# Performance work log

Measured on AMD Instinct MI355X. Metric: run time of the kernel, lower is better.

Reference implementation:

```python
import jax, jax.numpy as jnp
import numpy as np

B, S, F, D, K = 4096, 64, 8, 64, 16  # batch_size, seq_len, input_size, d_model, knns


def setup_inputs() -> dict:
    key = jax.random.key(0)
    ks = jax.random.split(key, 3)
    return {
        "x": jax.random.normal(ks[0], (B, S, F), jnp.float32),
        "W_emb": jax.random.normal(ks[1], (F, D), jnp.float32) / np.sqrt(F),
        "b_emb": jnp.zeros((D,), jnp.float32),
        "W_proj": jax.random.normal(ks[2], (D, F), jnp.float32) / np.sqrt(D),
        "b_proj": jnp.zeros((F,), jnp.float32),
    }


def reference(x, W_emb, b_emb, W_proj, b_proj):
    # enc_embedding
    x_enc = x @ W_emb + b_emb                       # [B,S,D]
    x_re = x_enc.reshape(B, S * D)                  # flatten per sample
    # batch self-similarity
    attn = jnp.einsum('bl,cl->bc', x_re, x_re) / np.sqrt(D * S)
    diag = jnp.eye(B, dtype=bool)
    attn = jnp.where(diag, -jnp.inf, attn)
    scores = jax.nn.softmax(attn, axis=-1)          # [B,B]
    # einsum('bd,bc->bd', x_re, scores) == x_re * scores.sum(-1)
    x_rec = x_re * jnp.sum(scores, axis=-1, keepdims=True)
    x_rec = x_rec.reshape(B, S, D)
    x_rec_proj = x_rec @ W_proj + b_proj            # [B,S,F]
    # top-k neighbor gather
    _, top_idx = jax.lax.top_k(scores, K)           # [B,K] int32
    gathered = x_rec_proj[top_idx]                  # [B,K,S,F]
    diff_1 = jnp.mean(jnp.diff(gathered, axis=1) ** 2)
    diff_2 = jnp.mean(jnp.diff(gathered, axis=2) ** 2)
    loss = jnp.mean((x_rec_proj - x) ** 2) + diff_1 + diff_2  # var == 2
    return loss, x_rec_proj
```

## Files before the change

### kernel.cpp

```cpp
#include <hip/hip_runtime.h>
#include <math.h>

#define NB 4096
#define NS 64
#define NF 8
#define ND 64
#define KL 512
#define NK 16

typedef _Float16 half8 __attribute__((ext_vector_type(8)));
typedef float    f32x4 __attribute__((ext_vector_type(4)));

#define GLD16(src, dst) \
  __builtin_amdgcn_global_load_lds((const __attribute__((address_space(1))) void*)(src), \
                                   (__attribute__((address_space(3))) void*)(dst), 16, 0, 0)

#define WAITVM(N) asm volatile("s_waitcnt vmcnt(" #N ")" ::: "memory")

__device__ __forceinline__ unsigned short f2bf_rne(float f) {
    unsigned v = __float_as_uint(f);
    return (unsigned short)((v + 0x7FFFu + ((v >> 16) & 1u)) >> 16);
}
__device__ __forceinline__ unsigned bf16key(float v, int col) {
    const unsigned u = f2bf_rne(v);
    const unsigned s = (u & 0x8000u) ? (~u & 0xFFFFu) : (u | 0x8000u);
    return (s << 12) | (unsigned)(4095 - col);
}

#define UPD2(M1, M2, K) { const unsigned k_ = (K); \
    if (k_ > M1) { M2 = M1; M1 = k_; } else if (k_ > M2) M2 = k_; }

__device__ __forceinline__ float blk_reduce(float v, float* red) {
    #pragma unroll
    for (int o = 32; o > 0; o >>= 1) v += __shfl_down(v, o, 64);
    const int t = threadIdx.x;
    __syncthreads();
    if ((t & 63) == 0) red[t >> 6] = v;
    __syncthreads();
    float r = 0.f;
    if (t == 0) r = red[0] + red[1] + red[2] + red[3];
    return r;
}

__global__ __launch_bounds__(64) void consts_kernel(
    const float* __restrict__ Wemb, const float* __restrict__ bemb,
    const float* __restrict__ Wp, const float* __restrict__ bp,
    float* __restrict__ cst, double* __restrict__ acc)
{
    __shared__ float sWe[NF * ND];
    __shared__ float sWp[ND * NF];
    __shared__ float sbe[ND];
    __shared__ float sbp[NF];
    const int t = threadIdx.x;
    #pragma unroll
    for (int i = 0; i < 12; ++i) acc[t + i * 64] = 0.0;
    #pragma unroll
    for (int i = 0; i < 8; ++i) { sWe[t + i * 64] = Wemb[t + i * 64]; sWp[t + i * 64] = Wp[t + i * 64]; }
    sbe[t] = bemb[t];
    if (t < NF) sbp[t] = bp[t];
    __syncthreads();
    const int f = t >> 3, f2 = t & 7;
    float g = 0.f, m = 0.f;
    #pragma unroll
    for (int d = 0; d < ND; ++d) {
        g += sWe[f * ND + d] * sWe[f2 * ND + d];
        m += sWe[f * ND + d] * sWp[d * NF + f2];
    }
    cst[t] = g;
    cst[64 + t] = m;
    if (t < NF) {
        float uu = 0.f, cc = 0.f;
        #pragma unroll
        for (int d = 0; d < ND; ++d) {
            uu += sWe[t * ND + d] * sbe[d];
            cc += sbe[d] * sWp[d * NF + t];
        }
        cst[128 + t] = uu;
        cst[136 + t] = cc + sbp[t];
    }
}

__global__ __launch_bounds__(256) void prep_kernel(
    const float* __restrict__ x, const float* __restrict__ cst,
    _Float16* __restrict__ X16, _Float16* __restrict__ Y16,
    float* __restrict__ proj, float* __restrict__ r, double* __restrict__ acc)
{
    __shared__ float sG[64], sM[64], su[8], sc[8];
    __shared__ float red[4];
    const int t = threadIdx.x, lane = t & 63, w = t >> 6;
    if (t < 64) sG[t] = cst[t];
    else if (t < 128) sM[t - 64] = cst[t];
    else if (t < 136) su[t - 128] = cst[t];
    else if (t < 144) sc[t - 136] = cst[t];
    __syncthreads();
    const int b = blockIdx.x * 4 + w;
    const size_t base = (size_t)b * KL + lane * 8;
    const f32x4 x0 = *(const f32x4*)&x[base];
    const f32x4 x1 = *(const f32x4*)&x[base + 4];
    float xv[8] = {x0[0], x0[1], x0[2], x0[3], x1[0], x1[1], x1[2], x1[3]};
    float yv[8], pv[8];
    #pragma unroll
    for (int f2 = 0; f2 < 8; ++f2) { yv[f2] = 0.f; pv[f2] = sc[f2]; }
    #pragma unroll
    for (int f = 0; f < 8; ++f)
        #pragma unroll
        for (int f2 = 0; f2 < 8; ++f2) {
            yv[f2] += xv[f] * sG[f * 8 + f2];
            pv[f2] += xv[f] * sM[f * 8 + f2];
        }
    half8 hx, hy;
    #pragma unroll
    for (int j = 0; j < 8; ++j) { hx[j] = (_Float16)xv[j]; hy[j] = (_Float16)yv[j]; }
    *(half8*)&X16[base] = hx;
    *(half8*)&Y16[base] = hy;
    *(f32x4*)&proj[base] = (f32x4){pv[0], pv[1], pv[2], pv[3]};
    *(f32x4*)&proj[base + 4] = (f32x4){pv[4], pv[5], pv[6], pv[7]};
    float rv = 0.f;
    #pragma unroll
    for (int f = 0; f < 8; ++f) rv += xv[f] * su[f];
    #pragma unroll
    for (int o = 32; o > 0; o >>= 1) rv += __shfl_down(rv, o, 64);
    if (lane == 0) r[b] = rv;
    float s1 = 0.f;
    #pragma unroll
    for (int j = 0; j < 8; ++j) { const float d = pv[j] - xv[j]; s1 += d * d; }
    const float tot = blk_reduce(s1, red);
    if (t == 0) atomicAdd(&acc[(size_t)(blockIdx.x & 31) * 8], (double)tot);
}

__global__ __launch_bounds__(256) void attn_gemm_kernel(
    const _Float16* __restrict__ Xf, const _Float16* __restrict__ Yf,
    const float* __restrict__ rvec, unsigned* __restrict__ cand)
{
    __shared__ __align__(16) char smem_raw[49152];
    _Float16* smem = (_Float16*)smem_raw;

    const int t = threadIdx.x;
    const int lane = t & 63, wid = t >> 6;
    const int wr = wid >> 1, wc = wid & 1;

    const int bid0 = blockIdx.x;
    const int bid = (bid0 & 7) * 66 + (bid0 >> 3);

    int it = (int)((sqrtf(8.0f * (float)bid + 1.0f) - 1.0f) * 0.5f);
    while ((it + 1) * (it + 2) / 2 <= bid) ++it;
    while (it * (it + 1) / 2 > bid) --it;
    const int jt = bid - it * (it + 1) / 2;
    const int i0 = it * 128, j0 = jt * 128;

    f32x4 acc[4][4];
    #pragma unroll
    for (int m = 0; m < 4; ++m)
        #pragma unroll
        for (int n = 0; n < 4; ++n) acc[m][n] = (f32x4){0.f, 0.f, 0.f, 0.f};

    const int lrow = lane & 15, g = lane >> 4;
    const int ksw = (g ^ ((lrow >> 1) & 3)) * 8;

    const int c0 = t, c1 = t + 256;
    const int r0 = c0 >> 2, r1 = c1 >> 2;
    const int cs0 = ((c0 & 3) ^ ((r0 >> 1) & 3)) * 8;
    const int cs1 = ((c1 & 3) ^ ((r1 >> 1) & 3)) * 8;
    const _Float16* pa0 = Xf + (size_t)(i0 + r0) * KL + cs0;
    const _Float16* pa1 = Xf + (size_t)(i0 + r1) * KL + cs1;
    const _Float16* pb0 = Yf + (size_t)(j0 + r0) * KL + cs0;
    const _Float16* pb1 = Yf + (size_t)(j0 + r1) * KL + cs1;
    _Float16* d0 = smem + c0 * 8;
    _Float16* d1 = smem + c1 * 8;

#define STG(BUF, KH) { \
    GLD16(pa0 + (KH), d0 + (BUF) * 8192); \
    GLD16(pa1 + (KH), d1 + (BUF) * 8192); \
    GLD16(pb0 + (KH), d0 + (BUF) * 8192 + 4096); \
    GLD16(pb1 + (KH), d1 + (BUF) * 8192 + 4096); }

    const int roA = wr * 2048 + lrow * 32 + ksw;
    const int roB = wc * 2048 + lrow * 32 + ksw;

#define COMPUTE(BUF) { \
    const _Float16* sA = smem + (BUF) * 8192; \
    const _Float16* sB = sA + 4096; \
    half8 fa[4], fb[4]; \
    _Pragma("unroll") \
    for (int m = 0; m < 4; ++m) { \
        fa[m] = *(const half8*)&sA[roA + m * 512]; \
        fb[m] = *(const half8*)&sB[roB + m * 512]; \
    } \
    __builtin_amdgcn_s_setprio(1); \
    _Pragma("unroll") \
    for (int m = 0; m < 4; ++m) \
        _Pragma("unroll") \
        for (int n = 0; n < 4; ++n) \
            acc[m][n] = __builtin_amdgcn_mfma_f32_16x16x32_f16(fa[m], fb[n], acc[m][n], 0, 0, 0); \
    __builtin_amdgcn_s_setprio(0); }

    STG(0, 0); STG(1, 32);
    pa0 += 64; pa1 += 64; pb0 += 64; pb1 += 64;
    #pragma unroll 1
    for (int io = 0; io < 4; ++io) {
        WAITVM(4); __builtin_amdgcn_s_barrier(); STG(2, 0);  COMPUTE(0);
        WAITVM(4); __builtin_amdgcn_s_barrier(); STG(0, 32); COMPUTE(1);
        WAITVM(4); __builtin_amdgcn_s_barrier(); STG(1, 64); COMPUTE(2);
        pa0 += 96; pa1 += 96; pb0 += 96; pb1 += 96;
    }
    WAITVM(4); __builtin_amdgcn_s_barrier(); STG(2, 0);  COMPUTE(0);
    WAITVM(4); __builtin_amdgcn_s_barrier(); STG(0, 32); COMPUTE(1);
    WAITVM(4); __builtin_amdgcn_s_barrier(); COMPUTE(2);
    WAITVM(0); __builtin_amdgcn_s_barrier(); COMPUTE(0);
#undef STG
#undef COMPUTE

    const int diag = (it == jt);

    float rj[4];
    #pragma unroll
    for (int n = 0; n < 4; ++n) rj[n] = rvec[j0 + wc * 64 + n * 16 + lrow];

    uint2* dp = (uint2*)smem_raw;
    uint2* mp = (uint2*)(smem_raw + 34816);

    __syncthreads();

    #pragma unroll
    for (int m = 0; m < 4; ++m)
        #pragma unroll
        for (int rr = 0; rr < 4; ++rr) {
            const int rl = wr * 64 + m * 16 + g * 4 + rr;
            const int i  = i0 + rl;
            unsigned m1 = 0u, m2 = 0u;
            #pragma unroll
            for (int n = 0; n < 4; ++n) {
                const int j = j0 + wc * 64 + n * 16 + lrow;
                unsigned key = bf16key(acc[m][n][rr] + rj[n], j);
                if (diag && i == j) key = 0u;
                UPD2(m1, m2, key)
            }
            uint2 pr; pr.x = m1; pr.y = m2;
            dp[(rl * 2 + wc) * 17 + lrow] = pr;
        }

    if (!diag) {
        #pragma unroll
        for (int n = 0; n < 4; ++n) {
            const int cl = wc * 64 + n * 16 + lrow;
            unsigned m1 = 0u, m2 = 0u;
            #pragma unroll
            for (int m = 0; m < 4; ++m) {
                const f32x4 riv = *(const f32x4*)&rvec[i0 + wr * 64 + m * 16 + g * 4];
                #pragma unroll
                for (int rr = 0; rr < 4; ++rr)
                    UPD2(m1, m2, bf16key(acc[m][n][rr] + riv[rr],
                                         i0 + wr * 64 + m * 16 + g * 4 + rr))
            }
            uint2 pr; pr.x = m1; pr.y = m2;
            mp[(cl * 2 + wr) * 4 + g] = pr;
        }
    }

    __syncthreads();

    {
        const int rl = t >> 1, p = t & 1;
        unsigned m1 = 0u, m2 = 0u;
        #pragma unroll
        for (int l = 0; l < 16; ++l) {
            const uint2 pr = dp[(rl * 2 + p) * 17 + l];
            UPD2(m1, m2, pr.x) UPD2(m1, m2, pr.y)
        }
        uint2 st; st.x = m1; st.y = m2;
        *(uint2*)(cand + (size_t)(i0 + rl) * 128 + (size_t)(jt * 2 + p) * 2) = st;
    }

    if (!diag) {
        const int cl = t >> 1, q = t & 1;
        unsigned m1 = 0u, m2 = 0u;
        #pragma unroll
        for (int gg = 0; gg < 4; ++gg) {
            const uint2 pr = mp[(cl * 2 + q) * 4 + gg];
            UPD2(m1, m2, pr.x) UPD2(m1, m2, pr.y)
        }
        uint2 st; st.x = m1; st.y = m2;
        *(uint2*)(cand + (size_t)(j0 + cl) * 128 + (size_t)(it * 2 + q) * 2) = st;
    }
}

__global__ __launch_bounds__(256) void topk_diffs_kernel(
    const unsigned* __restrict__ cand, const float* __restrict__ proj,
    double* __restrict__ acc)
{
    const int t = threadIdx.x, lane = t & 63, w = t >> 6;
    const int b = blockIdx.x * 4 + w;
    const uint2 kk = *(const uint2*)(cand + (size_t)b * 128 + lane * 2);
    unsigned k0 = kk.x, k1 = kk.y;

    float s1 = 0.f, s2 = 0.f;
    float prev[8];

    for (int k = 0; k < NK; ++k) {
        unsigned bv = k0 > k1 ? k0 : k1;
        #pragma unroll
        for (int o = 1; o <= 32; o <<= 1)
            bv = max(bv, (unsigned)__shfl_xor((int)bv, o, 64));
        const int idx = 4095 - (int)(bv & 0xFFFu);

        const float* pp = proj + (size_t)idx * 512 + lane * 8;
        const f32x4 a0 = *(const f32x4*)pp;
        const f32x4 a1 = *(const f32x4*)(pp + 4);
        float cur[8] = {a0[0], a0[1], a0[2], a0[3], a1[0], a1[1], a1[2], a1[3]};
        if (k) {
            #pragma unroll
            for (int j = 0; j < 8; ++j) { const float d = cur[j] - prev[j]; s1 += d * d; }
        }
        if (lane < 63) {
            const f32x4 n0 = *(const f32x4*)(pp + 8);
            const f32x4 n1 = *(const f32x4*)(pp + 12);
            const float nxt[8] = {n0[0], n0[1], n0[2], n0[3], n1[0], n1[1], n1[2], n1[3]};
            #pragma unroll
            for (int j = 0; j < 8; ++j) { const float d = nxt[j] - cur[j]; s2 += d * d; }
        }
        #pragma unroll
        for (int j = 0; j < 8; ++j) prev[j] = cur[j];

        if (k0 == bv) k0 = 0u;
        if (k1 == bv) k1 = 0u;
    }

    #pragma unroll
    for (int o = 32; o > 0; o >>= 1) { s1 += __shfl_down(s1, o, 64); s2 += __shfl_down(s2, o, 64); }
    if (lane == 0) {
        const size_t slot = (size_t)(blockIdx.x & 31) * 8;
        atomicAdd(&acc[(size_t)32 * 8 + slot], (double)s1);
        atomicAdd(&acc[(size_t)64 * 8 + slot], (double)s2);
    }
}

__global__ void finalize_kernel(const double* __restrict__ acc, float* __restrict__ out) {
    if (threadIdx.x == 0) {
        double s0 = 0.0, s1 = 0.0, s2 = 0.0;
        #pragma unroll
        for (int i = 0; i < 32; ++i) {
            s0 += acc[(size_t)i * 8];
            s1 += acc[(size_t)(32 + i) * 8];
            s2 += acc[(size_t)(64 + i) * 8];
        }
        out[0] = (float)(s0 / 2097152.0 + s1 / 31457280.0 + s2 / 33030144.0);
    }
}

extern "C" void kernel_launch(void* const* d_in, const int* in_sizes, int n_in,
                              void* d_out, int out_size, void* d_ws, size_t ws_size,
                              hipStream_t stream) {
    const float* x    = (const float*)d_in[0];
    const float* Wemb = (const float*)d_in[1];
    const float* bemb = (const float*)d_in[2];
    const float* Wp   = (const float*)d_in[3];
    const float* bp   = (const float*)d_in[4];
    float* out  = (float*)d_out;
    float* proj = out + 1;

    char* ws = (char*)d_ws;
    _Float16* X16 = (_Float16*)ws;
    _Float16* Y16 = (_Float16*)(ws + ((size_t)4 << 20));
    unsigned* cand = (unsigned*)(ws + ((size_t)8 << 20));
    float*  cst   = (float*)(ws + ((size_t)10 << 20));
    float*  rvec  = (float*)(ws + ((size_t)10 << 20) + 4096);
    double* acc   = (double*)(ws + ((size_t)10 << 20) + 65536);

    consts_kernel<<<1, 64, 0, stream>>>(Wemb, bemb, Wp, bp, cst, acc);
    prep_kernel<<<NB / 4, 256, 0, stream>>>(x, cst, X16, Y16, proj, rvec, acc);
    attn_gemm_kernel<<<(32 * 33) / 2, 256, 0, stream>>>(X16, Y16, rvec, cand);
    topk_diffs_kernel<<<NB / 4, 256, 0, stream>>>(cand, proj, acc);
    finalize_kernel<<<1, 64, 0, stream>>>(acc, out);
}
```

Measured before the change: 70.97 us.

## Replace triangular symmetric tiling with full square grid in attention GEMM

Result: no change. 69.59 us (-1.9%).

```diff
diff --git a/kernel.cpp b/kernel.cpp
--- a/kernel.cpp
+++ b/kernel.cpp
@@ -140,12 +140,8 @@
     const int wr = wid >> 1, wc = wid & 1;
 
     const int bid0 = blockIdx.x;
-    const int bid = (bid0 & 7) * 66 + (bid0 >> 3);
-
-    int it = (int)((sqrtf(8.0f * (float)bid + 1.0f) - 1.0f) * 0.5f);
-    while ((it + 1) * (it + 2) / 2 <= bid) ++it;
-    while (it * (it + 1) / 2 > bid) --it;
-    const int jt = bid - it * (it + 1) / 2;
+    const int bid = (bid0 & 7) * 128 + (bid0 >> 3);
+    const int it = bid >> 5, jt = bid & 31;
     const int i0 = it * 128, j0 = jt * 128;
 
     f32x4 acc[4][4];
@@ -217,7 +213,6 @@
     for (int n = 0; n < 4; ++n) rj[n] = rvec[j0 + wc * 64 + n * 16 + lrow];
 
     uint2* dp = (uint2*)smem_raw;
-    uint2* mp = (uint2*)(smem_raw + 34816);
 
     __syncthreads();
 
@@ -239,24 +234,6 @@
             dp[(rl * 2 + wc) * 17 + lrow] = pr;
         }
 
-    if (!diag) {
-        #pragma unroll
-        for (int n = 0; n < 4; ++n) {
-            const int cl = wc * 64 + n * 16 + lrow;
-            unsigned m1 = 0u, m2 = 0u;
-            #pragma unroll
-            for (int m = 0; m < 4; ++m) {
-                const f32x4 riv = *(const f32x4*)&rvec[i0 + wr * 64 + m * 16 + g * 4];
-                #pragma unroll
-                for (int rr = 0; rr < 4; ++rr)
-                    UPD2(m1, m2, bf16key(acc[m][n][rr] + riv[rr],
-                                         i0 + wr * 64 + m * 16 + g * 4 + rr))
-            }
-            uint2 pr; pr.x = m1; pr.y = m2;
-            mp[(cl * 2 + wr) * 4 + g] = pr;
-        }
-    }
-
     __syncthreads();
 
     {
@@ -269,18 +246,6 @@
         }
         uint2 st; st.x = m1; st.y = m2;
         *(uint2*)(cand + (size_t)(i0 + rl) * 128 + (size_t)(jt * 2 + p) * 2) = st;
-    }
-
-    if (!diag) {
-        const int cl = t >> 1, q = t & 1;
-        unsigned m1 = 0u, m2 = 0u;
-        #pragma unroll
-        for (int gg = 0; gg < 4; ++gg) {
-            const uint2 pr = mp[(cl * 2 + q) * 4 + gg];
-            UPD2(m1, m2, pr.x) UPD2(m1, m2, pr.y)
-        }
-        uint2 st; st.x = m1; st.y = m2;
-        *(uint2*)(cand + (size_t)(j0 + cl) * 128 + (size_t)(it * 2 + q) * 2) = st;
     }
 }
 
@@ -368,7 +333,7 @@
 
     consts_kernel<<<1, 64, 0, stream>>>(Wemb, bemb, Wp, bp, cst, acc);
     prep_kernel<<<NB / 4, 256, 0, stream>>>(x, cst, X16, Y16, proj, rvec, acc);
-    attn_gemm_kernel<<<(32 * 33) / 2, 256, 0, stream>>>(X16, Y16, rvec, cand);
+    attn_gemm_kernel<<<1024, 256, 0, stream>>>(X16, Y16, rvec, cand);
     topk_diffs_kernel<<<NB / 4, 256, 0, stream>>>(cand, proj, acc);
     finalize_kernel<<<1, 64, 0, stream>>>(acc, out);
 }
```
